# Performance work log

Hardware: AMD Instinct MI355X
Metric: run time of the kernel (lower is better)

The kernel has to match this reference:

```python
import jax, jax.numpy as jnp
import numpy as np

B, S, H, F, E, TOP_K = 4, 2048, 768, 3072, 8, 2


def setup_inputs() -> dict:
    key = jax.random.key(0)
    ks = jax.random.split(key, 6)
    x = jax.random.normal(ks[0], (B, S, H), dtype=jnp.float32)
    Wr = jax.random.normal(ks[1], (E, H), dtype=jnp.float32) * 0.02
    Wi = jax.random.normal(ks[2], (E, F, H), dtype=jnp.float32) * 0.02
    bi = jnp.zeros((E, F), dtype=jnp.float32)
    Wo = jax.random.normal(ks[3], (E, H, F), dtype=jnp.float32) * 0.02
    bo = jnp.zeros((E, H), dtype=jnp.float32)
    return {"x": x, "Wr": Wr, "Wi": Wi, "bi": bi, "Wo": Wo, "bo": bo}


def reference(x, Wr, Wi, bi, Wo, bo):
    # x: [B, S, H] -> tokens [T, H]
    xf = x.reshape(-1, x.shape[-1])  # [T, H]

    # Router: linear (no bias), eval mode (no noise), temperature=1.0
    router_logits = jnp.einsum('th,eh->te', xf, Wr)  # [T, E]
    topk_vals, topk_idx = jax.lax.top_k(router_logits, TOP_K)  # [T, K]
    routing_weights = jax.nn.softmax(topk_vals, axis=-1)  # normalize over top-k

    # All experts on all tokens (forward_all_experts, parallel computation)
    h = jnp.einsum('th,efh->etf', xf, Wi) + bi[:, None, :]  # [E, T, F]
    h = jax.nn.gelu(h, approximate=False)  # BERT gelu (erf)
    expert_out = jnp.einsum('etf,ehf->eth', h, Wo) + bo[:, None, :]  # [E, T, H]
    expert_out = jnp.transpose(expert_out, (1, 0, 2))  # [T, E, H]

    # Gather top-k expert outputs per token and combine with routing weights
    gathered = jnp.take_along_axis(expert_out, topk_idx[:, :, None], axis=1)  # [T, K, H]
    out = jnp.einsum('tk,tkh->th', routing_weights, gathered)
    return out.reshape(x.shape)
```

## Files before the change

kernel.cpp:

```cpp
#include <hip/hip_runtime.h>
#include <hip/hip_bf16.h>
#include <cstdint>
#include <cstddef>

#define T_TOK 8192
#define HDIM  768
#define FDIM  3072
#define NEXP  8

typedef __attribute__((ext_vector_type(8))) __bf16 bf16x8;
typedef __attribute__((ext_vector_type(4))) float  f32x4;

static __device__ __forceinline__ f32x4 mfma16(bf16x8 a, bf16x8 b, f32x4 c) {
  return __builtin_amdgcn_mfma_f32_16x16x32_bf16(a, b, c, 0, 0, 0);
}

static __device__ __forceinline__ unsigned short f2b(float f) {
  return __builtin_bit_cast(unsigned short, (__bf16)f);
}

static __device__ __forceinline__ float gelu_f(float x) {
  float x2 = x * x;
  float y = x * (0.7978845608f + 0.0356774081f * x2);
  float ay = __builtin_fabsf(y);
  float z = __builtin_amdgcn_exp2f(ay * -2.885390082f);
  float t = (1.0f - z) * __builtin_amdgcn_rcpf(1.0f + z);
  t = __builtin_copysignf(t, y);
  return 0.5f * x * (1.0f + t);
}

static constexpr size_t OFF_XB   = 0;
static constexpr size_t OFF_WIB  = OFF_XB  + (size_t)T_TOK * HDIM * 2;
static constexpr size_t OFF_WOB  = OFF_WIB + (size_t)NEXP * FDIM * HDIM * 2;
static constexpr size_t OFF_HBUF = OFF_WOB + (size_t)NEXP * HDIM * FDIM * 2;
static constexpr size_t OFF_META = OFF_HBUF + (size_t)2 * T_TOK * FDIM * 2;
static constexpr size_t OFF_TOKE = OFF_META + 256;
static constexpr size_t OFF_TOKW = OFF_TOKE + 65536;
static constexpr size_t OFF_PTOK = OFF_TOKW + 65536;
static constexpr size_t OFF_PW   = OFF_PTOK + 65536;
static constexpr size_t OFF_TILE = OFF_PW + 65536;
static constexpr size_t OFF_STAGE = 0;

__global__ __launch_bounds__(256) void cvt_kernel(const float* __restrict__ s,
                                                  unsigned short* __restrict__ d, int n4) {
  int i = blockIdx.x * 256 + threadIdx.x;
  int stride = gridDim.x * 256;
  for (; i < n4; i += stride) {
    float4 v = ((const float4*)s)[i];
    ushort4 o;
    o.x = f2b(v.x); o.y = f2b(v.y); o.z = f2b(v.z); o.w = f2b(v.w);
    ((ushort4*)d)[i] = o;
  }
}

__global__ __launch_bounds__(256) void router_kernel(const float* __restrict__ x,
                                                     const float* __restrict__ Wr,
                                                     int* __restrict__ tok_e,
                                                     float* __restrict__ tok_w,
                                                     unsigned short* __restrict__ xb) {
  __shared__ float wr[NEXP * HDIM];
  int tid = threadIdx.x;
  for (int i = tid; i < NEXP * HDIM; i += 256) wr[i] = Wr[i];
  __syncthreads();
  int lane = tid & 63;
  int wv = tid >> 6;
  int t = blockIdx.x * 4 + wv;
  const float* xr = x + (size_t)t * HDIM;
  unsigned short* xbr = xb + (size_t)t * HDIM;
  float p[NEXP];
#pragma unroll
  for (int e = 0; e < NEXP; ++e) p[e] = 0.f;
  for (int j = 0; j < HDIM / 64; ++j) {
    float xv = xr[j * 64 + lane];
    xbr[j * 64 + lane] = f2b(xv);
#pragma unroll
    for (int e = 0; e < NEXP; ++e) p[e] += xv * wr[e * HDIM + j * 64 + lane];
  }
#pragma unroll
  for (int e = 0; e < NEXP; ++e) {
    float v = p[e];
    for (int off = 32; off; off >>= 1) v += __shfl_xor(v, off);
    p[e] = v;
  }
  if (lane == 0) {
    float v0 = -1e30f, v1 = -1e30f; int i0 = 0, i1 = 0;
#pragma unroll
    for (int e = 0; e < NEXP; ++e) {
      float v = p[e];
      if (v > v0) { v1 = v0; i1 = i0; v0 = v; i0 = e; }
      else if (v > v1) { v1 = v; i1 = e; }
    }
    float ew = expf(v1 - v0);
    float w0 = 1.0f / (1.0f + ew);
    float w1 = ew * w0;
    tok_e[t * 2 + 0] = i0; tok_w[t * 2 + 0] = w0;
    tok_e[t * 2 + 1] = i1; tok_w[t * 2 + 1] = w1;
  }
}

__global__ __launch_bounds__(256) void count_kernel(const int* __restrict__ tok_e,
                                                    int* __restrict__ counts) {
  __shared__ int h[NEXP];
  int tid = threadIdx.x;
  if (tid < NEXP) h[tid] = 0;
  __syncthreads();
  int i = blockIdx.x * 256 + tid;
  atomicAdd(&h[tok_e[i]], 1);
  __syncthreads();
  if (tid < NEXP && h[tid] > 0) atomicAdd(&counts[tid], h[tid]);
}

__global__ void scan_build_kernel(const int* __restrict__ counts, int* __restrict__ basep,
                                  int* __restrict__ tileA_e, int* __restrict__ tileA_mt,
                                  int* __restrict__ ntiles) {
  if (threadIdx.x != 0 || blockIdx.x != 0) return;
  int s = 0;
  for (int e = 0; e < NEXP; ++e) { basep[e] = s; s += counts[e]; }
  int na = 0;
  for (int e = 0; e < NEXP; ++e) {
    int nmt = (counts[e] + 127) >> 7;
    for (int m = 0; m < nmt; ++m) { tileA_e[na] = e; tileA_mt[na] = m; ++na; }
  }
  ntiles[1] = na;
}

__global__ __launch_bounds__(256) void scatter_kernel(const int* __restrict__ tok_e,
                                                      const float* __restrict__ tok_w,
                                                      const int* __restrict__ base,
                                                      int* __restrict__ cursor,
                                                      int* __restrict__ pair_tok,
                                                      float* __restrict__ pair_w) {
  __shared__ int h[NEXP], bstart[NEXP];
  int tid = threadIdx.x;
  if (tid < NEXP) h[tid] = 0;
  __syncthreads();
  int i = blockIdx.x * 256 + tid;
  int e = tok_e[i];
  int r = atomicAdd(&h[e], 1);
  __syncthreads();
  if (tid < NEXP) bstart[tid] = (h[tid] > 0) ? atomicAdd(&cursor[tid], h[tid]) : 0;
  __syncthreads();
  int pos = base[e] + bstart[e] + r;
  pair_tok[pos] = i;
  pair_w[pos] = tok_w[i];
}

template <int MODE>
__global__ __launch_bounds__(256, 3) void moe_gemm128(
    const unsigned short* __restrict__ abase,
    const unsigned short* __restrict__ wbase,
    const float* __restrict__ bias,
    const int* __restrict__ counts, const int* __restrict__ base,
    const int* __restrict__ pair_tok, const float* __restrict__ pair_w,
    const int* __restrict__ tileA_e, const int* __restrict__ tileA_mt,
    const int* __restrict__ ntiles,
    unsigned short* __restrict__ hbuf, float* __restrict__ stage) {
  constexpr int K  = MODE ? FDIM : HDIM;
  constexpr int N  = MODE ? HDIM : FDIM;
  constexpr int NT = K / 64;

  const int xcd = blockIdx.x & 7;
  const int slot = blockIdx.x >> 3;
  const int mtl = slot % 18;
  const int nt = slot / 18;
  const int ntl = ntiles[1];
  const int q = ntl >> 3, r = ntl & 7;
  const int cnt = q + (xcd < r ? 1 : 0);
  if (mtl >= cnt) return;
  const int gt = xcd * q + (xcd < r ? xcd : r) + mtl;
  const int e = tileA_e[gt];
  const int mt = tileA_mt[gt];
  const int ne = counts[e];
  const int pb = base[e];

  extern __shared__ char smem[];

  const int tid = threadIdx.x;
  const int lane = tid & 63;
  const int wv = tid >> 6;
  const int wm = wv >> 1;
  const int wn = wv & 1;
  const int l15 = lane & 15;
  const int lkb = (lane >> 4) * 16;

  const int crow = tid >> 3;
  const int ck = tid & 7;
  const int swz = (ck ^ (crow & 7)) * 16;
  const char* aS[4]; const char* bS[4];
#pragma unroll
  for (int c = 0; c < 4; ++c) {
    int gr = mt * 128 + c * 32 + crow; if (gr > ne - 1) gr = ne - 1;
    if constexpr (MODE == 0) {
      int tok = pair_tok[pb + gr] >> 1;
      aS[c] = (const char*)abase + (size_t)tok * (HDIM * 2) + swz;
    } else {
      aS[c] = (const char*)abase + (size_t)(pb + gr) * (FDIM * 2) + swz;
    }
    int br = nt * 128 + c * 32 + crow;
    bS[c] = (const char*)wbase + ((size_t)e * N * K + (size_t)br * K) * 2 + swz;
  }

  auto STAGE = [&](int t) {
    if (t < NT) {
#pragma unroll
      for (int c = 0; c < 4; ++c) {
        __builtin_amdgcn_global_load_lds(
            (const __attribute__((address_space(1))) void*)(aS[c] + t * 128),
            (__attribute__((address_space(3))) void*)(smem + c * 4096 + tid * 16), 16, 0, 0);
        __builtin_amdgcn_global_load_lds(
            (const __attribute__((address_space(1))) void*)(bS[c] + t * 128),
            (__attribute__((address_space(3))) void*)(smem + 16384 + c * 4096 + tid * 16),
            16, 0, 0);
      }
    }
  };

  f32x4 acc[4][4];
#pragma unroll
  for (int mf = 0; mf < 4; ++mf)
#pragma unroll
    for (int nf = 0; nf < 4; ++nf) acc[mf][nf] = (f32x4){0.f, 0.f, 0.f, 0.f};

  STAGE(0);
  asm volatile("s_waitcnt vmcnt(0)" ::: "memory");
  __builtin_amdgcn_s_barrier();

  for (int t = 0; t < NT; ++t) {
    bf16x8 aF[8], bF[8];
#pragma unroll
    for (int mf = 0; mf < 4; ++mf)
#pragma unroll
      for (int kh = 0; kh < 2; ++kh) {
        int lr = wm * 64 + mf * 16 + l15;
        aF[mf * 2 + kh] =
            *(const bf16x8*)(smem + lr * 128 + ((kh * 64 + lkb) ^ ((lr & 7) << 4)));
      }
#pragma unroll
    for (int nf = 0; nf < 4; ++nf)
#pragma unroll
      for (int kh = 0; kh < 2; ++kh) {
        int lb = wn * 64 + nf * 16 + l15;
        bF[nf * 2 + kh] =
            *(const bf16x8*)(smem + 16384 + lb * 128 + ((kh * 64 + lkb) ^ ((lb & 7) << 4)));
      }
    asm volatile("s_waitcnt lgkmcnt(0)" ::: "memory");
    __builtin_amdgcn_sched_barrier(0);
    __builtin_amdgcn_s_barrier();
    STAGE(t + 1);
    __builtin_amdgcn_sched_barrier(0);
    __builtin_amdgcn_s_setprio(1);
#pragma unroll
    for (int mf = 0; mf < 4; ++mf)
#pragma unroll
      for (int nf = 0; nf < 4; ++nf)
#pragma unroll
        for (int kh = 0; kh < 2; ++kh)
          acc[mf][nf] = mfma16(aF[mf * 2 + kh], bF[nf * 2 + kh], acc[mf][nf]);
    __builtin_amdgcn_s_setprio(0);
    __builtin_amdgcn_sched_barrier(0);
    asm volatile("s_waitcnt vmcnt(0)" ::: "memory");
    __builtin_amdgcn_s_barrier();
  }

  if constexpr (MODE == 0) {
    const float* be = bias + (size_t)e * FDIM;
    float bv[4];
#pragma unroll
    for (int nf = 0; nf < 4; ++nf) bv[nf] = be[nt * 128 + wn * 64 + nf * 16 + l15];
#pragma unroll
    for (int mf = 0; mf < 4; ++mf)
#pragma unroll
      for (int rr = 0; rr < 4; ++rr) {
        int row = mt * 128 + wm * 64 + mf * 16 + (lane >> 4) * 4 + rr;
        if (row < ne) {
          unsigned short* hr = hbuf + (size_t)(pb + row) * FDIM + nt * 128 + wn * 64 + l15;
#pragma unroll
          for (int nf = 0; nf < 4; ++nf)
            hr[nf * 16] = f2b(gelu_f(acc[mf][nf][rr] + bv[nf]));
        }
      }
  } else {
    const float* be = bias + (size_t)e * HDIM;
    float bv[4];
#pragma unroll
    for (int nf = 0; nf < 4; ++nf) bv[nf] = be[nt * 128 + wn * 64 + nf * 16 + l15];
#pragma unroll
    for (int mf = 0; mf < 4; ++mf)
#pragma unroll
      for (int rr = 0; rr < 4; ++rr) {
        int row = mt * 128 + wm * 64 + mf * 16 + (lane >> 4) * 4 + rr;
        if (row < ne) {
          int p = pb + row;
          int ts = pair_tok[p];
          float w = pair_w[p];
          float* sr = stage + (size_t)ts * HDIM + nt * 128 + wn * 64 + l15;
#pragma unroll
          for (int nf = 0; nf < 4; ++nf)
            sr[nf * 16] = (acc[mf][nf][rr] + bv[nf]) * w;
        }
      }
  }
}

__global__ __launch_bounds__(256) void combine_kernel(const float* __restrict__ stage,
                                                      float* __restrict__ out) {
  const int n4 = T_TOK * HDIM / 4;
  int i = blockIdx.x * 256 + threadIdx.x;
  int stride = gridDim.x * 256;
  const float4* s = (const float4*)stage;
  float4* o = (float4*)out;
  for (; i < n4; i += stride) {
    int t = i / (HDIM / 4);
    int h = i - t * (HDIM / 4);
    float4 a = s[(size_t)t * (HDIM / 2) + h];
    float4 b = s[(size_t)t * (HDIM / 2) + (HDIM / 4) + h];
    float4 rr; rr.x = a.x + b.x; rr.y = a.y + b.y; rr.z = a.z + b.z; rr.w = a.w + b.w;
    o[i] = rr;
  }
}

extern "C" void kernel_launch(void* const* d_in, const int* in_sizes, int n_in,
                              void* d_out, int out_size, void* d_ws, size_t ws_size,
                              hipStream_t stream) {
  const float* x  = (const float*)d_in[0];
  const float* Wr = (const float*)d_in[1];
  const float* Wi = (const float*)d_in[2];
  const float* bi = (const float*)d_in[3];
  const float* Wo = (const float*)d_in[4];
  const float* bo = (const float*)d_in[5];
  float* out = (float*)d_out;
  char* ws = (char*)d_ws;

  unsigned short* xb   = (unsigned short*)(ws + OFF_XB);
  unsigned short* wib  = (unsigned short*)(ws + OFF_WIB);
  unsigned short* wob  = (unsigned short*)(ws + OFF_WOB);
  unsigned short* hbuf = (unsigned short*)(ws + OFF_HBUF);
  int*   counts   = (int*)(ws + OFF_META);
  int*   basep    = (int*)(ws + OFF_META + 64);
  int*   cursor   = (int*)(ws + OFF_META + 128);
  int*   tok_e    = (int*)(ws + OFF_TOKE);
  float* tok_w    = (float*)(ws + OFF_TOKW);
  int*   pair_tok = (int*)(ws + OFF_PTOK);
  float* pair_w   = (float*)(ws + OFF_PW);
  int*   tileA_e  = (int*)(ws + OFF_TILE);
  int*   tileA_mt = (int*)(ws + OFF_TILE + 1024);
  int*   ntiles   = (int*)(ws + OFF_TILE + 2048);
  float* stage    = (float*)(ws + OFF_STAGE);

  hipFuncSetAttribute((const void*)&moe_gemm128<0>,
                      hipFuncAttributeMaxDynamicSharedMemorySize, 32768);
  hipFuncSetAttribute((const void*)&moe_gemm128<1>,
                      hipFuncAttributeMaxDynamicSharedMemorySize, 32768);

  hipMemsetAsync(ws + OFF_META, 0, 256, stream);

  router_kernel<<<T_TOK / 4, 256, 0, stream>>>(x, Wr, tok_e, tok_w, xb);
  cvt_kernel<<<2048, 256, 0, stream>>>(Wi, wib, NEXP * FDIM * HDIM / 4);
  cvt_kernel<<<2048, 256, 0, stream>>>(Wo, wob, NEXP * HDIM * FDIM / 4);

  count_kernel<<<64, 256, 0, stream>>>(tok_e, counts);
  scan_build_kernel<<<1, 64, 0, stream>>>(counts, basep, tileA_e, tileA_mt, ntiles);
  scatter_kernel<<<64, 256, 0, stream>>>(tok_e, tok_w, basep, cursor, pair_tok, pair_w);

  moe_gemm128<0><<<8 * 18 * (FDIM / 128), 256, 32768, stream>>>(
      xb, wib, bi, counts, basep, pair_tok, pair_w, tileA_e, tileA_mt, ntiles, hbuf, nullptr);
  moe_gemm128<1><<<8 * 18 * (HDIM / 128), 256, 32768, stream>>>(
      hbuf, wob, bo, counts, basep, pair_tok, pair_w, tileA_e, tileA_mt, ntiles, nullptr, stage);

  combine_kernel<<<2048, 256, 0, stream>>>(stage, out);
}
```

Before: 303.3 us.

## Widen MoE GEMM tile to 128x256 with per-wave 128x64 and split-K reads

Changes the grouped GEMM block tile from 128x128 to 128x256. Each of the four waves now owns the full 128 rows and a 64-column slice, using 8x4 accumulator fragments. LDS reads are split into two k-halves so the first half's MFMAs overlap the second half's fragment loads. The goal is more MFMA work per byte of LDS and global traffic and fewer blocks re-reading the A tile. In exchange the accumulators double, launch bounds drop to 2 blocks per CU, LDS grows to 48KB, and the grid has fewer blocks (notably only 3 N-tiles for the second GEMM).

After: 292.7 us. -3.5%, faster.

```diff
diff --git a/kernel.cpp b/kernel.cpp
--- a/kernel.cpp
+++ b/kernel.cpp
@@ -146,7 +146,7 @@
 }
 
 template <int MODE>
-__global__ __launch_bounds__(256, 3) void moe_gemm128(
+__global__ __launch_bounds__(256, 2) void moe_gemm128(
     const unsigned short* __restrict__ abase,
     const unsigned short* __restrict__ wbase,
     const float* __restrict__ bias,
@@ -177,16 +177,14 @@
 
   const int tid = threadIdx.x;
   const int lane = tid & 63;
-  const int wv = tid >> 6;
-  const int wm = wv >> 1;
-  const int wn = wv & 1;
+  const int wn = tid >> 6;
   const int l15 = lane & 15;
   const int lkb = (lane >> 4) * 16;
 
   const int crow = tid >> 3;
   const int ck = tid & 7;
   const int swz = (ck ^ (crow & 7)) * 16;
-  const char* aS[4]; const char* bS[4];
+  const char* aS[4];
 #pragma unroll
   for (int c = 0; c < 4; ++c) {
     int gr = mt * 128 + c * 32 + crow; if (gr > ne - 1) gr = ne - 1;
@@ -196,66 +194,72 @@
     } else {
       aS[c] = (const char*)abase + (size_t)(pb + gr) * (FDIM * 2) + swz;
     }
-    int br = nt * 128 + c * 32 + crow;
-    bS[c] = (const char*)wbase + ((size_t)e * N * K + (size_t)br * K) * 2 + swz;
-  }
+  }
+  const char* bS = (const char*)wbase +
+                   ((size_t)e * N * K + (size_t)(nt * 256 + crow) * K) * 2 + swz;
 
   auto STAGE = [&](int t) {
     if (t < NT) {
 #pragma unroll
-      for (int c = 0; c < 4; ++c) {
+      for (int c = 0; c < 4; ++c)
         __builtin_amdgcn_global_load_lds(
             (const __attribute__((address_space(1))) void*)(aS[c] + t * 128),
             (__attribute__((address_space(3))) void*)(smem + c * 4096 + tid * 16), 16, 0, 0);
+#pragma unroll
+      for (int c = 0; c < 8; ++c)
         __builtin_amdgcn_global_load_lds(
-            (const __attribute__((address_space(1))) void*)(bS[c] + t * 128),
+            (const __attribute__((address_space(1))) void*)(bS + (size_t)c * (32 * K * 2) + t * 128),
             (__attribute__((address_space(3))) void*)(smem + 16384 + c * 4096 + tid * 16),
             16, 0, 0);
-      }
     }
   };
 
-  f32x4 acc[4][4];
-#pragma unroll
-  for (int mf = 0; mf < 4; ++mf)
+  f32x4 acc[8][4];
+#pragma unroll
+  for (int mf = 0; mf < 8; ++mf)
 #pragma unroll
     for (int nf = 0; nf < 4; ++nf) acc[mf][nf] = (f32x4){0.f, 0.f, 0.f, 0.f};
+
+  auto RD = [&](int kh, bf16x8* aF, bf16x8* bF) {
+#pragma unroll
+    for (int mf = 0; mf < 8; ++mf) {
+      int lr = mf * 16 + l15;
+      aF[mf] = *(const bf16x8*)(smem + lr * 128 + ((kh * 64 + lkb) ^ ((lr & 7) << 4)));
+    }
+#pragma unroll
+    for (int nf = 0; nf < 4; ++nf) {
+      int lb = wn * 64 + nf * 16 + l15;
+      bF[nf] = *(const bf16x8*)(smem + 16384 + lb * 128 + ((kh * 64 + lkb) ^ ((lb & 7) << 4)));
+    }
+  };
+  auto MM = [&](const bf16x8* aF, const bf16x8* bF) {
+#pragma unroll
+    for (int mf = 0; mf < 8; ++mf)
+#pragma unroll
+      for (int nf = 0; nf < 4; ++nf)
+        acc[mf][nf] = mfma16(aF[mf], bF[nf], acc[mf][nf]);
+  };
 
   STAGE(0);
   asm volatile("s_waitcnt vmcnt(0)" ::: "memory");
   __builtin_amdgcn_s_barrier();
 
   for (int t = 0; t < NT; ++t) {
-    bf16x8 aF[8], bF[8];
-#pragma unroll
-    for (int mf = 0; mf < 4; ++mf)
-#pragma unroll
-      for (int kh = 0; kh < 2; ++kh) {
-        int lr = wm * 64 + mf * 16 + l15;
-        aF[mf * 2 + kh] =
-            *(const bf16x8*)(smem + lr * 128 + ((kh * 64 + lkb) ^ ((lr & 7) << 4)));
-      }
-#pragma unroll
-    for (int nf = 0; nf < 4; ++nf)
-#pragma unroll
-      for (int kh = 0; kh < 2; ++kh) {
-        int lb = wn * 64 + nf * 16 + l15;
-        bF[nf * 2 + kh] =
-            *(const bf16x8*)(smem + 16384 + lb * 128 + ((kh * 64 + lkb) ^ ((lb & 7) << 4)));
-      }
+    bf16x8 aF[8], bF[4];
+    RD(0, aF, bF);
+    asm volatile("s_waitcnt lgkmcnt(0)" ::: "memory");
+    __builtin_amdgcn_sched_barrier(0);
+    __builtin_amdgcn_s_setprio(1);
+    MM(aF, bF);
+    __builtin_amdgcn_s_setprio(0);
+    RD(1, aF, bF);
     asm volatile("s_waitcnt lgkmcnt(0)" ::: "memory");
     __builtin_amdgcn_sched_barrier(0);
     __builtin_amdgcn_s_barrier();
     STAGE(t + 1);
     __builtin_amdgcn_sched_barrier(0);
     __builtin_amdgcn_s_setprio(1);
-#pragma unroll
-    for (int mf = 0; mf < 4; ++mf)
-#pragma unroll
-      for (int nf = 0; nf < 4; ++nf)
-#pragma unroll
-        for (int kh = 0; kh < 2; ++kh)
-          acc[mf][nf] = mfma16(aF[mf * 2 + kh], bF[nf * 2 + kh], acc[mf][nf]);
+    MM(aF, bF);
     __builtin_amdgcn_s_setprio(0);
     __builtin_amdgcn_sched_barrier(0);
     asm volatile("s_waitcnt vmcnt(0)" ::: "memory");
@@ -266,14 +270,14 @@
     const float* be = bias + (size_t)e * FDIM;
     float bv[4];
 #pragma unroll
-    for (int nf = 0; nf < 4; ++nf) bv[nf] = be[nt * 128 + wn * 64 + nf * 16 + l15];
-#pragma unroll
-    for (int mf = 0; mf < 4; ++mf)
+    for (int nf = 0; nf < 4; ++nf) bv[nf] = be[nt * 256 + wn * 64 + nf * 16 + l15];
+#pragma unroll
+    for (int mf = 0; mf < 8; ++mf)
 #pragma unroll
       for (int rr = 0; rr < 4; ++rr) {
-        int row = mt * 128 + wm * 64 + mf * 16 + (lane >> 4) * 4 + rr;
+        int row = mt * 128 + mf * 16 + (lane >> 4) * 4 + rr;
         if (row < ne) {
-          unsigned short* hr = hbuf + (size_t)(pb + row) * FDIM + nt * 128 + wn * 64 + l15;
+          unsigned short* hr = hbuf + (size_t)(pb + row) * FDIM + nt * 256 + wn * 64 + l15;
 #pragma unroll
           for (int nf = 0; nf < 4; ++nf)
             hr[nf * 16] = f2b(gelu_f(acc[mf][nf][rr] + bv[nf]));
@@ -283,17 +287,17 @@
     const float* be = bias + (size_t)e * HDIM;
     float bv[4];
 #pragma unroll
-    for (int nf = 0; nf < 4; ++nf) bv[nf] = be[nt * 128 + wn * 64 + nf * 16 + l15];
-#pragma unroll
-    for (int mf = 0; mf < 4; ++mf)
+    for (int nf = 0; nf < 4; ++nf) bv[nf] = be[nt * 256 + wn * 64 + nf * 16 + l15];
+#pragma unroll
+    for (int mf = 0; mf < 8; ++mf)
 #pragma unroll
       for (int rr = 0; rr < 4; ++rr) {
-        int row = mt * 128 + wm * 64 + mf * 16 + (lane >> 4) * 4 + rr;
+        int row = mt * 128 + mf * 16 + (lane >> 4) * 4 + rr;
         if (row < ne) {
           int p = pb + row;
           int ts = pair_tok[p];
           float w = pair_w[p];
-          float* sr = stage + (size_t)ts * HDIM + nt * 128 + wn * 64 + l15;
+          float* sr = stage + (size_t)ts * HDIM + nt * 256 + wn * 64 + l15;
 #pragma unroll
           for (int nf = 0; nf < 4; ++nf)
             sr[nf * 16] = (acc[mf][nf][rr] + bv[nf]) * w;
@@ -348,9 +352,9 @@
   float* stage    = (float*)(ws + OFF_STAGE);
 
   hipFuncSetAttribute((const void*)&moe_gemm128<0>,
-                      hipFuncAttributeMaxDynamicSharedMemorySize, 32768);
+                      hipFuncAttributeMaxDynamicSharedMemorySize, 49152);
   hipFuncSetAttribute((const void*)&moe_gemm128<1>,
-                      hipFuncAttributeMaxDynamicSharedMemorySize, 32768);
+                      hipFuncAttributeMaxDynamicSharedMemorySize, 49152);
 
   hipMemsetAsync(ws + OFF_META, 0, 256, stream);
 
@@ -362,9 +366,9 @@
   scan_build_kernel<<<1, 64, 0, stream>>>(counts, basep, tileA_e, tileA_mt, ntiles);
   scatter_kernel<<<64, 256, 0, stream>>>(tok_e, tok_w, basep, cursor, pair_tok, pair_w);
 
-  moe_gemm128<0><<<8 * 18 * (FDIM / 128), 256, 32768, stream>>>(
+  moe_gemm128<0><<<8 * 18 * (FDIM / 256), 256, 49152, stream>>>(
       xb, wib, bi, counts, basep, pair_tok, pair_w, tileA_e, tileA_mt, ntiles, hbuf, nullptr);
-  moe_gemm128<1><<<8 * 18 * (HDIM / 128), 256, 32768, stream>>>(
+  moe_gemm128<1><<<8 * 18 * (HDIM / 256), 256, 49152, stream>>>(
       hbuf, wob, bo, counts, basep, pair_tok, pair_w, tileA_e, tileA_mt, ntiles, nullptr, stage);
 
   combine_kernel<<<2048, 256, 0, stream>>>(stage, out);
```
